# Optimization experiments

Measured on AMD Instinct MI355X. Metric: run time of the kernel, lower is better.

Reference implementation:

```python
import jax, jax.numpy as jnp
import numpy as np

N_NODES = 50000
N_EDGES = 800000
D_IN = 16


def gcn_conv(x, edge_index, W, b, n_nodes):
    """PyG GCNConv: x' = D^{-1/2} (A + I) D^{-1/2} X W + b (add_self_loops=True)."""
    h = x @ W  # [N, d_out] - transform before propagate (small d => cheaper)
    src = jnp.concatenate([edge_index[0], jnp.arange(n_nodes)])  # add self-loops
    dst = jnp.concatenate([edge_index[1], jnp.arange(n_nodes)])
    deg = jax.ops.segment_sum(jnp.ones_like(dst, dtype=h.dtype), dst,
                              num_segments=n_nodes)  # in-degree incl. self-loop
    deg_inv_sqrt = jnp.where(deg > 0, jax.lax.rsqrt(deg), 0.0)
    norm = deg_inv_sqrt[src] * deg_inv_sqrt[dst]  # [E+N]
    msg = h[src] * norm[:, None]                  # gather + scale
    out = jax.ops.segment_sum(msg, dst, num_segments=n_nodes)  # scatter-add
    return out + b


def setup_inputs() -> dict:
    key = jax.random.key(0)
    ks = jax.random.split(key, 16)
    d = D_IN
    x = jax.random.normal(ks[0], (N_NODES, d), dtype=jnp.float32)
    edge_index = jax.random.randint(ks[1], (2, N_EDGES), 0, N_NODES, dtype=jnp.int64)

    def glorot(k, fan_in, fan_out):
        s = (6.0 / (fan_in + fan_out)) ** 0.5
        return jax.random.uniform(k, (fan_in, fan_out), jnp.float32, -s, s)

    return {
        "x": x,
        "edge_index": edge_index,
        "W1": glorot(ks[2], d, 2 * d),      "b1": jnp.zeros((2 * d,), jnp.float32),
        "W2": glorot(ks[3], 2 * d, 4 * d),  "b2": jnp.zeros((4 * d,), jnp.float32),
        "W3": glorot(ks[4], 4 * d, 8 * d),  "b3": jnp.zeros((8 * d,), jnp.float32),
        "Wl1": glorot(ks[5], 8 * d, 4 * d), "bl1": jnp.zeros((4 * d,), jnp.float32),
        "Wl2": glorot(ks[6], 4 * d, 2 * d), "bl2": jnp.zeros((2 * d,), jnp.float32),
        "Wl3": glorot(ks[7], 2 * d, d),     "bl3": jnp.zeros((d,), jnp.float32),
    }


def reference(x, edge_index, W1, b1, W2, b2, W3, b3, Wl1, bl1, Wl2, bl2, Wl3, bl3):
    n = x.shape[0]
    # note: original applies relu twice per conv; relu is idempotent
    out = jax.nn.relu(gcn_conv(x, edge_index, W1, b1, n))
    out = jax.nn.relu(gcn_conv(out, edge_index, W2, b2, n))
    out = jax.nn.relu(gcn_conv(out, edge_index, W3, b3, n))
    out = jax.nn.relu(out @ Wl1 + bl1)
    out = jax.nn.relu(out @ Wl2 + bl2)
    out = jax.nn.relu(out @ Wl3 + bl3)
    return out
```

## Files before the change

kernel.cpp:

```cpp
#include <hip/hip_runtime.h>

#define TPB 256
#define TE  2048
#define MAXB 6144

typedef _Float16 half_t;
typedef _Float16 half4 __attribute__((ext_vector_type(4)));
typedef _Float16 half8 __attribute__((ext_vector_type(8)));
typedef float float8v __attribute__((ext_vector_type(8)));

static inline int cdiv(int a, int b) { return (a + b - 1) / b; }


__global__ void k_zero_int(int* p, int n) {
    int i = blockIdx.x * blockDim.x + threadIdx.x;
    if (i < n) p[i] = 0;
}

__global__ void k_bhist(const int* __restrict__ dst, int* __restrict__ gcnt,
                        int e, int nb) {
    __shared__ int lc[256];
    for (int t = threadIdx.x; t < nb; t += TPB) lc[t] = 0;
    __syncthreads();
    for (int i = blockIdx.x * TPB + threadIdx.x; i < e; i += gridDim.x * TPB)
        atomicAdd(&lc[dst[i] >> 8], 1);
    __syncthreads();
    for (int t = threadIdx.x; t < nb; t += TPB) {
        int v = lc[t];
        if (v) atomicAdd(&gcnt[t], v);
    }
}

__global__ void k_bscan(const int* __restrict__ gcnt, int* __restrict__ bstart,
                        int* __restrict__ bcur, int nb, int e) {
    __shared__ int s[256];
    int t = threadIdx.x;
    int v = (t < nb) ? gcnt[t] : 0;
    s[t] = v;
    __syncthreads();
    for (int d = 1; d < 256; d <<= 1) {
        int x = (t >= d) ? s[t - d] : 0;
        __syncthreads();
        s[t] += x;
        __syncthreads();
    }
    if (t < nb) { int ex = s[t] - v; bstart[t] = ex; bcur[t] = ex; }
    if (t == 0) bstart[nb] = e;
}

__global__ void __launch_bounds__(TPB)
k_binscatter(const int* __restrict__ src, const int* __restrict__ dst,
             int* __restrict__ bcur, unsigned int* __restrict__ gbuf,
             int e, int nb) {
    __shared__ int lcnt[256], loffs[256], lcur[256], gres[256];
    __shared__ int ss[256];
    __shared__ unsigned int ldata[TE];
    const int base = blockIdx.x * TE;
    const int cnt = min(TE, e - base);
    for (int t = threadIdx.x; t < nb; t += TPB) lcnt[t] = 0;
    __syncthreads();

    unsigned int myv[TE / TPB];
    int myb[TE / TPB];
#pragma unroll
    for (int k = 0; k < TE / TPB; ++k) {
        int j = threadIdx.x + k * TPB;
        if (j < cnt) {
            int d = dst[base + j], s = src[base + j];
            int b = d >> 8;
            myv[k] = ((unsigned)b << 24) | ((unsigned)(d & 255) << 16) | (unsigned)s;
            myb[k] = b;
            atomicAdd(&lcnt[b], 1);
        } else myb[k] = -1;
    }
    __syncthreads();
    {
        int t = threadIdx.x;
        int v = (t < nb) ? lcnt[t] : 0;
        ss[t] = v;
        __syncthreads();
        for (int d = 1; d < 256; d <<= 1) {
            int x = (t >= d) ? ss[t - d] : 0;
            __syncthreads();
            ss[t] += x;
            __syncthreads();
        }
        if (t < nb) { loffs[t] = ss[t] - v; lcur[t] = ss[t] - v; }
    }
    __syncthreads();
    for (int t = threadIdx.x; t < nb; t += TPB)
        if (lcnt[t]) gres[t] = atomicAdd(&bcur[t], lcnt[t]);
#pragma unroll
    for (int k = 0; k < TE / TPB; ++k) {
        if (myb[k] >= 0) {
            int p = atomicAdd(&lcur[myb[k]], 1);
            ldata[p] = myv[k];
        }
    }
    __syncthreads();
    for (int j = threadIdx.x; j < cnt; j += TPB) {
        unsigned int v = ldata[j];
        int b = v >> 24;
        gbuf[gres[b] + (j - loffs[b])] = v & 0xFFFFFFu;
    }
}

__global__ void __launch_bounds__(TPB)
k_csr(const unsigned int* __restrict__ gbuf, const int* __restrict__ bstart,
      int* __restrict__ offs, float* __restrict__ dinv, int* __restrict__ ssrc,
      int n, int e) {
    __shared__ int cnt[256], loffs2[256], lcur2[256], ss[256];
    __shared__ int stage[MAXB];
    const int b = blockIdx.x;
    const int s0 = bstart[b], s1 = bstart[b + 1];
    const int m = s1 - s0;
    cnt[threadIdx.x] = 0;
    __syncthreads();
    for (int j = threadIdx.x; j < m; j += TPB)
        atomicAdd(&cnt[(gbuf[s0 + j] >> 16) & 255], 1);
    __syncthreads();
    {
        int t = threadIdx.x;
        int v = cnt[t];
        ss[t] = v;
        __syncthreads();
        for (int d = 1; d < 256; d <<= 1) {
            int x = (t >= d) ? ss[t - d] : 0;
            __syncthreads();
            ss[t] += x;
            __syncthreads();
        }
        loffs2[t] = ss[t] - v;
        lcur2[t] = ss[t] - v;
        int node = b * 256 + t;
        if (node < n) {
            offs[node] = s0 + loffs2[t];
            dinv[node] = rsqrtf((float)v + 1.0f);
        }
    }
    __syncthreads();
    for (int j = threadIdx.x; j < m; j += TPB) {
        unsigned int v = gbuf[s0 + j];
        int p = atomicAdd(&lcur2[(v >> 16) & 255], 1);
        stage[p] = (int)(v & 0xFFFFu);
    }
    __syncthreads();
    for (int j = threadIdx.x; j < m; j += TPB) ssrc[s0 + j] = stage[j];
    if (b == 0 && threadIdx.x == 0) offs[n] = e;
}


__global__ void k_scale(const float* __restrict__ x, const float* __restrict__ dinv,
                        half_t* __restrict__ G, int n) {
    int idx = blockIdx.x * blockDim.x + threadIdx.x;
    if (idx >= n * 2) return;
    float d = dinv[idx >> 1];
    float8v v = ((const float8v*)x)[idx];
    half8 h;
#pragma unroll
    for (int q = 0; q < 8; ++q) h[q] = (half_t)(v[q] * d);
    ((half8*)G)[idx] = h;
}

template<int D>
__global__ void __launch_bounds__(TPB)
k_gather(const int* __restrict__ offs, const int* __restrict__ ssrc,
         const half_t* __restrict__ G, const float* __restrict__ dinv,
         float* __restrict__ A, int n) {
    constexpr int C = D / 8;
    int idx = blockIdx.x * blockDim.x + threadIdx.x;
    if (idx >= n * C) return;
    int i = idx / C;
    int c = idx & (C - 1);
    const half8* Grow = (const half8*)G;
    half8 hs = Grow[(size_t)i * C + c];
    float8v acc;
#pragma unroll
    for (int q = 0; q < 8; ++q) acc[q] = (float)hs[q];
    int s0 = offs[i], s1 = offs[i + 1];
    int j = s0;
    for (; j + 1 < s1; j += 2) {
        int sa = ssrc[j], sb = ssrc[j + 1];
        half8 ga = Grow[(size_t)sa * C + c];
        half8 gb = Grow[(size_t)sb * C + c];
#pragma unroll
        for (int q = 0; q < 8; ++q) acc[q] += (float)ga[q] + (float)gb[q];
    }
    if (j < s1) {
        half8 ga = Grow[(size_t)ssrc[j] * C + c];
#pragma unroll
        for (int q = 0; q < 8; ++q) acc[q] += (float)ga[q];
    }
    float di = dinv[i];
#pragma unroll
    for (int q = 0; q < 8; ++q) acc[q] *= di;
    ((float8v*)A)[(size_t)i * C + c] = acc;
}

template<int DI, int DO, int R, bool SCALE, bool OUT_HALF>
__global__ void __launch_bounds__(TPB, 2)
k_gemm(const float* __restrict__ A, const float* __restrict__ W,
       const float* __restrict__ b, const float* __restrict__ dinv,
       void* __restrict__ outp, int n) {
    constexpr int CT = DO / 4;
    constexpr int RT = TPB / CT;
    constexpr int TM = RT * R;
    constexpr int K4 = DI / 4;
    constexpr int PX = K4 + 1;
    __shared__ float4 sW4[DI * CT];
    __shared__ float4 sX4[TM * PX];
    const int tid = threadIdx.x;

    const float4* Wg = (const float4*)W;
    for (int t = tid; t < DI * CT; t += TPB) sW4[t] = Wg[t];

    const int r0 = blockIdx.x * TM;
    const float4* Ag = (const float4*)A;
    for (int t = tid; t < TM * K4; t += TPB) {
        int r = t / K4, k4 = t - r * K4;
        int row = r0 + r;
        sX4[r * PX + k4] = (row < n) ? Ag[(size_t)row * K4 + k4]
                                     : make_float4(0.f, 0.f, 0.f, 0.f);
    }
    __syncthreads();

    const int c = tid & (CT - 1);
    const int rg = tid / CT;
    const int rbase = rg * R;
    float4 acc[R];
#pragma unroll
    for (int r = 0; r < R; ++r) acc[r] = make_float4(0.f, 0.f, 0.f, 0.f);

#pragma unroll 2
    for (int k4 = 0; k4 < K4; ++k4) {
        float4 xv[R];
#pragma unroll
        for (int r = 0; r < R; ++r) xv[r] = sX4[(rbase + r) * PX + k4];
#pragma unroll
        for (int kk = 0; kk < 4; ++kk) {
            float4 wv = sW4[(k4 * 4 + kk) * CT + c];
#pragma unroll
            for (int r = 0; r < R; ++r) {
                float xs = (kk == 0) ? xv[r].x : (kk == 1) ? xv[r].y
                         : (kk == 2) ? xv[r].z : xv[r].w;
                acc[r].x += xs * wv.x; acc[r].y += xs * wv.y;
                acc[r].z += xs * wv.z; acc[r].w += xs * wv.w;
            }
        }
    }

    float4 bc = ((const float4*)b)[c];
#pragma unroll
    for (int r = 0; r < R; ++r) {
        int row = r0 + rbase + r;
        if (row < n) {
            float4 o;
            o.x = fmaxf(acc[r].x + bc.x, 0.f);
            o.y = fmaxf(acc[r].y + bc.y, 0.f);
            o.z = fmaxf(acc[r].z + bc.z, 0.f);
            o.w = fmaxf(acc[r].w + bc.w, 0.f);
            if (SCALE) {
                float d = dinv[row];
                o.x *= d; o.y *= d; o.z *= d; o.w *= d;
            }
            if (OUT_HALF) {
                half4 h;
                h.x = (half_t)o.x; h.y = (half_t)o.y;
                h.z = (half_t)o.z; h.w = (half_t)o.w;
                ((half4*)outp)[(size_t)row * CT + c] = h;
            } else {
                ((float4*)outp)[(size_t)row * CT + c] = o;
            }
        }
    }
}

extern "C" void kernel_launch(void* const* d_in, const int* in_sizes, int n_in,
                              void* d_out, int out_size, void* d_ws, size_t ws_size,
                              hipStream_t stream) {
    const float* x   = (const float*)d_in[0];
    const int*   ei  = (const int*)d_in[1];
    const float* W1  = (const float*)d_in[2];
    const float* bb1 = (const float*)d_in[3];
    const float* W2  = (const float*)d_in[4];
    const float* bb2 = (const float*)d_in[5];
    const float* W3  = (const float*)d_in[6];
    const float* bb3 = (const float*)d_in[7];
    const float* Wl1 = (const float*)d_in[8];
    const float* bl1 = (const float*)d_in[9];
    const float* Wl2 = (const float*)d_in[10];
    const float* bl2 = (const float*)d_in[11];
    const float* Wl3 = (const float*)d_in[12];
    const float* bl3 = (const float*)d_in[13];
    float* out = (float*)d_out;

    const int n = in_sizes[0] / 16;
    const int e = in_sizes[1] / 2;
    const int* src = ei;
    const int* dst = ei + e;
    const int nb = cdiv(n, 256);

    char* p = (char*)d_ws;
    auto alloc = [&](size_t bytes) {
        char* r = p;
        p += (bytes + 255) & ~(size_t)255;
        return r;
    };
    float*        dinv   = (float*)        alloc((size_t)n * 4);
    int*          offs   = (int*)          alloc((size_t)(n + 1) * 4);
    int*          gcnt   = (int*)          alloc(256 * 4);
    int*          bstart = (int*)          alloc(257 * 4);
    int*          bcur   = (int*)          alloc(256 * 4);
    unsigned int* gbuf   = (unsigned int*) alloc((size_t)e * 4);
    int*          ssrc   = (int*)          alloc((size_t)e * 4);
    half_t*       H1     = (half_t*)       alloc((size_t)n * 64 * 2);
    half_t*       H2     = (half_t*)       alloc((size_t)n * 64 * 2);
    float*        A      = (float*)        alloc((size_t)n * 64 * 4);
    float*        X3     = (float*)        alloc((size_t)n * 128 * 4);
    float*        T1     = A;
    float*        T2     = (float*)H1;

    k_zero_int<<<1, 256, 0, stream>>>(gcnt, nb);
    k_bhist<<<512, TPB, 0, stream>>>(dst, gcnt, e, nb);
    k_bscan<<<1, 256, 0, stream>>>(gcnt, bstart, bcur, nb, e);
    k_binscatter<<<cdiv(e, TE), TPB, 0, stream>>>(src, dst, bcur, gbuf, e, nb);
    k_csr<<<nb, TPB, 0, stream>>>(gbuf, bstart, offs, dinv, ssrc, n, e);

    k_scale<<<cdiv(n * 2, TPB), TPB, 0, stream>>>(x, dinv, H1, n);
    k_gather<16><<<cdiv(n * 2, TPB), TPB, 0, stream>>>(offs, ssrc, H1, dinv, A, n);
    k_gemm<16, 32, 4, true, true><<<cdiv(n, 128), TPB, 0, stream>>>(A, W1, bb1, dinv, H2, n);

    k_gather<32><<<cdiv(n * 4, TPB), TPB, 0, stream>>>(offs, ssrc, H2, dinv, A, n);
    k_gemm<32, 64, 4, true, true><<<cdiv(n, 64), TPB, 0, stream>>>(A, W2, bb2, dinv, H1, n);

    k_gather<64><<<cdiv(n * 8, TPB), TPB, 0, stream>>>(offs, ssrc, H1, dinv, A, n);
    k_gemm<64, 128, 4, false, false><<<cdiv(n, 32), TPB, 0, stream>>>(A, W3, bb3, nullptr, X3, n);

    k_gemm<128, 64, 2, false, false><<<cdiv(n, 32), TPB, 0, stream>>>(X3, Wl1, bl1, nullptr, T1, n);
    k_gemm<64, 32, 2, false, false><<<cdiv(n, 64), TPB, 0, stream>>>(T1, Wl2, bl2, nullptr, T2, n);
    k_gemm<32, 16, 2, false, false><<<cdiv(n, 128), TPB, 0, stream>>>(T2, Wl3, bl3, nullptr, out, n);
}
```

Measured before the change: 231.6 us.

## Fuse neighbor gather into conv GEMM and fuse three MLP head layers

Each GCN layer's gather-aggregate now runs inside the GEMM kernel: every thread aggregates one 8-wide chunk of a row straight into shared memory, so the fp32 intermediate A is never written to or read back from global memory. The third conv now writes fp16 output, and a new fused head kernel runs all three linear+ReLU layers per 64-row tile with fp16 weights in shared memory. This drops several launches and large fp32 round trips. In exchange, the gather now runs with the GEMM tiling and occupancy, and the head layers lose some precision from the fp16 storage.

```diff
diff --git a/kernel.cpp b/kernel.cpp
--- a/kernel.cpp
+++ b/kernel.cpp
@@ -162,65 +162,59 @@
     ((half8*)G)[idx] = h;
 }
 
-template<int D>
-__global__ void __launch_bounds__(TPB)
-k_gather(const int* __restrict__ offs, const int* __restrict__ ssrc,
-         const half_t* __restrict__ G, const float* __restrict__ dinv,
-         float* __restrict__ A, int n) {
-    constexpr int C = D / 8;
-    int idx = blockIdx.x * blockDim.x + threadIdx.x;
-    if (idx >= n * C) return;
-    int i = idx / C;
-    int c = idx & (C - 1);
-    const half8* Grow = (const half8*)G;
-    half8 hs = Grow[(size_t)i * C + c];
-    float8v acc;
-#pragma unroll
-    for (int q = 0; q < 8; ++q) acc[q] = (float)hs[q];
-    int s0 = offs[i], s1 = offs[i + 1];
-    int j = s0;
-    for (; j + 1 < s1; j += 2) {
-        int sa = ssrc[j], sb = ssrc[j + 1];
-        half8 ga = Grow[(size_t)sa * C + c];
-        half8 gb = Grow[(size_t)sb * C + c];
-#pragma unroll
-        for (int q = 0; q < 8; ++q) acc[q] += (float)ga[q] + (float)gb[q];
-    }
-    if (j < s1) {
-        half8 ga = Grow[(size_t)ssrc[j] * C + c];
-#pragma unroll
-        for (int q = 0; q < 8; ++q) acc[q] += (float)ga[q];
-    }
-    float di = dinv[i];
-#pragma unroll
-    for (int q = 0; q < 8; ++q) acc[q] *= di;
-    ((float8v*)A)[(size_t)i * C + c] = acc;
-}
-
 template<int DI, int DO, int R, bool SCALE, bool OUT_HALF>
 __global__ void __launch_bounds__(TPB, 2)
-k_gemm(const float* __restrict__ A, const float* __restrict__ W,
-       const float* __restrict__ b, const float* __restrict__ dinv,
+k_conv(const int* __restrict__ offs, const int* __restrict__ ssrc,
+       const half_t* __restrict__ G, const float* __restrict__ dinv,
+       const float* __restrict__ W, const float* __restrict__ b,
        void* __restrict__ outp, int n) {
     constexpr int CT = DO / 4;
     constexpr int RT = TPB / CT;
     constexpr int TM = RT * R;
     constexpr int K4 = DI / 4;
     constexpr int PX = K4 + 1;
+    constexpr int C  = DI / 8;
+    static_assert(TM * C == TPB, "gather/gemm tile mismatch");
     __shared__ float4 sW4[DI * CT];
     __shared__ float4 sX4[TM * PX];
     const int tid = threadIdx.x;
+    const int r0 = blockIdx.x * TM;
 
     const float4* Wg = (const float4*)W;
     for (int t = tid; t < DI * CT; t += TPB) sW4[t] = Wg[t];
 
-    const int r0 = blockIdx.x * TM;
-    const float4* Ag = (const float4*)A;
-    for (int t = tid; t < TM * K4; t += TPB) {
-        int r = t / K4, k4 = t - r * K4;
-        int row = r0 + r;
-        sX4[r * PX + k4] = (row < n) ? Ag[(size_t)row * K4 + k4]
-                                     : make_float4(0.f, 0.f, 0.f, 0.f);
+    {
+        int gr = tid / C;
+        int gc = tid - gr * C;
+        int row = r0 + gr;
+        float8v acc;
+#pragma unroll
+        for (int q = 0; q < 8; ++q) acc[q] = 0.f;
+        if (row < n) {
+            const half8* Grow = (const half8*)G;
+            half8 hs = Grow[(size_t)row * C + gc];
+#pragma unroll
+            for (int q = 0; q < 8; ++q) acc[q] = (float)hs[q];
+            int s0 = offs[row], s1 = offs[row + 1];
+            int j = s0;
+            for (; j + 1 < s1; j += 2) {
+                int sa = ssrc[j], sb = ssrc[j + 1];
+                half8 ga = Grow[(size_t)sa * C + gc];
+                half8 gb = Grow[(size_t)sb * C + gc];
+#pragma unroll
+                for (int q = 0; q < 8; ++q) acc[q] += (float)ga[q] + (float)gb[q];
+            }
+            if (j < s1) {
+                half8 ga = Grow[(size_t)ssrc[j] * C + gc];
+#pragma unroll
+                for (int q = 0; q < 8; ++q) acc[q] += (float)ga[q];
+            }
+            float di = dinv[row];
+#pragma unroll
+            for (int q = 0; q < 8; ++q) acc[q] *= di;
+        }
+        sX4[gr * PX + 2 * gc]     = make_float4(acc[0], acc[1], acc[2], acc[3]);
+        sX4[gr * PX + 2 * gc + 1] = make_float4(acc[4], acc[5], acc[6], acc[7]);
     }
     __syncthreads();
 
@@ -271,6 +265,122 @@
             } else {
                 ((float4*)outp)[(size_t)row * CT + c] = o;
             }
+        }
+    }
+}
+
+__global__ void __launch_bounds__(256, 2)
+k_head(const half_t* __restrict__ X,
+       const float* __restrict__ W1, const float* __restrict__ b1,
+       const float* __restrict__ W2, const float* __restrict__ b2,
+       const float* __restrict__ W3, const float* __restrict__ b3,
+       float* __restrict__ out, int n) {
+    __shared__ half_t hW1[128 * 64];
+    __shared__ half_t hW2[64 * 32];
+    __shared__ half_t hW3[32 * 16];
+    __shared__ float h1[64 * 65];
+    __shared__ float h2[64 * 33];
+    const int tid = threadIdx.x;
+    const int r0 = blockIdx.x * 64;
+
+    for (int t = tid; t < 128 * 64; t += 256) hW1[t] = (half_t)W1[t];
+    for (int t = tid; t < 64 * 32; t += 256) hW2[t] = (half_t)W2[t];
+    for (int t = tid; t < 32 * 16; t += 256) hW3[t] = (half_t)W3[t];
+    __syncthreads();
+
+    {
+        const int c4 = tid & 15;
+        const int rowg = tid >> 4;
+        const half8* Xr = (const half8*)X;
+        float acc[4][4];
+#pragma unroll
+        for (int r = 0; r < 4; ++r)
+#pragma unroll
+            for (int j = 0; j < 4; ++j) acc[r][j] = 0.f;
+        for (int k8 = 0; k8 < 16; ++k8) {
+            half8 xh[4];
+#pragma unroll
+            for (int r = 0; r < 4; ++r) {
+                int row = r0 + rowg * 4 + r;
+                if (row < n) xh[r] = Xr[(size_t)row * 16 + k8];
+                else { half8 z; for (int q = 0; q < 8; ++q) z[q] = (half_t)0.f; xh[r] = z; }
+            }
+#pragma unroll
+            for (int q = 0; q < 8; ++q) {
+                int k = k8 * 8 + q;
+                half4 w = *(const half4*)&hW1[k * 64 + c4 * 4];
+                float w0 = (float)w.x, w1 = (float)w.y, w2 = (float)w.z, w3 = (float)w.w;
+#pragma unroll
+                for (int r = 0; r < 4; ++r) {
+                    float xs = (float)xh[r][q];
+                    acc[r][0] += xs * w0; acc[r][1] += xs * w1;
+                    acc[r][2] += xs * w2; acc[r][3] += xs * w3;
+                }
+            }
+        }
+        float4 bc = ((const float4*)b1)[c4];
+#pragma unroll
+        for (int r = 0; r < 4; ++r) {
+            int rl = rowg * 4 + r;
+            h1[rl * 65 + c4 * 4 + 0] = fmaxf(acc[r][0] + bc.x, 0.f);
+            h1[rl * 65 + c4 * 4 + 1] = fmaxf(acc[r][1] + bc.y, 0.f);
+            h1[rl * 65 + c4 * 4 + 2] = fmaxf(acc[r][2] + bc.z, 0.f);
+            h1[rl * 65 + c4 * 4 + 3] = fmaxf(acc[r][3] + bc.w, 0.f);
+        }
+    }
+    __syncthreads();
+
+    {
+        const int c4 = tid & 7;
+        const int rowg = tid >> 3;
+        float acc[2][4];
+#pragma unroll
+        for (int r = 0; r < 2; ++r)
+#pragma unroll
+            for (int j = 0; j < 4; ++j) acc[r][j] = 0.f;
+#pragma unroll 4
+        for (int k = 0; k < 64; ++k) {
+            half4 w = *(const half4*)&hW2[k * 32 + c4 * 4];
+            float w0 = (float)w.x, w1 = (float)w.y, w2 = (float)w.z, w3 = (float)w.w;
+#pragma unroll
+            for (int r = 0; r < 2; ++r) {
+                float xs = h1[(rowg * 2 + r) * 65 + k];
+                acc[r][0] += xs * w0; acc[r][1] += xs * w1;
+                acc[r][2] += xs * w2; acc[r][3] += xs * w3;
+            }
+        }
+        float4 bc = ((const float4*)b2)[c4];
+#pragma unroll
+        for (int r = 0; r < 2; ++r) {
+            int rl = rowg * 2 + r;
+            h2[rl * 33 + c4 * 4 + 0] = fmaxf(acc[r][0] + bc.x, 0.f);
+            h2[rl * 33 + c4 * 4 + 1] = fmaxf(acc[r][1] + bc.y, 0.f);
+            h2[rl * 33 + c4 * 4 + 2] = fmaxf(acc[r][2] + bc.z, 0.f);
+            h2[rl * 33 + c4 * 4 + 3] = fmaxf(acc[r][3] + bc.w, 0.f);
+        }
+    }
+    __syncthreads();
+
+    {
+        const int c4 = tid & 3;
+        const int rl = tid >> 2;
+        float a0 = 0.f, a1 = 0.f, a2 = 0.f, a3 = 0.f;
+#pragma unroll 4
+        for (int k = 0; k < 32; ++k) {
+            half4 w = *(const half4*)&hW3[k * 16 + c4 * 4];
+            float xs = h2[rl * 33 + k];
+            a0 += xs * (float)w.x; a1 += xs * (float)w.y;
+            a2 += xs * (float)w.z; a3 += xs * (float)w.w;
+        }
+        int row = r0 + rl;
+        if (row < n) {
+            float4 bc = ((const float4*)b3)[c4];
+            float4 o;
+            o.x = fmaxf(a0 + bc.x, 0.f);
+            o.y = fmaxf(a1 + bc.y, 0.f);
+            o.z = fmaxf(a2 + bc.z, 0.f);
+            o.w = fmaxf(a3 + bc.w, 0.f);
+            ((float4*)out)[(size_t)row * 4 + c4] = o;
         }
     }
 }
@@ -314,11 +424,8 @@
     unsigned int* gbuf   = (unsigned int*) alloc((size_t)e * 4);
     int*          ssrc   = (int*)          alloc((size_t)e * 4);
     half_t*       H1     = (half_t*)       alloc((size_t)n * 64 * 2);
-    half_t*       H2     = (half_t*)       alloc((size_t)n * 64 * 2);
-    float*        A      = (float*)        alloc((size_t)n * 64 * 4);
-    float*        X3     = (float*)        alloc((size_t)n * 128 * 4);
-    float*        T1     = A;
-    float*        T2     = (float*)H1;
+    half_t*       H2     = (half_t*)       alloc((size_t)n * 32 * 2);
+    half_t*       X3h    = (half_t*)       alloc((size_t)n * 128 * 2);
 
     k_zero_int<<<1, 256, 0, stream>>>(gcnt, nb);
     k_bhist<<<512, TPB, 0, stream>>>(dst, gcnt, e, nb);
@@ -327,16 +434,12 @@
     k_csr<<<nb, TPB, 0, stream>>>(gbuf, bstart, offs, dinv, ssrc, n, e);
 
     k_scale<<<cdiv(n * 2, TPB), TPB, 0, stream>>>(x, dinv, H1, n);
-    k_gather<16><<<cdiv(n * 2, TPB), TPB, 0, stream>>>(offs, ssrc, H1, dinv, A, n);
-    k_gemm<16, 32, 4, true, true><<<cdiv(n, 128), TPB, 0, stream>>>(A, W1, bb1, dinv, H2, n);
-
-    k_gather<32><<<cdiv(n * 4, TPB), TPB, 0, stream>>>(offs, ssrc, H2, dinv, A, n);
-    k_gemm<32, 64, 4, true, true><<<cdiv(n, 64), TPB, 0, stream>>>(A, W2, bb2, dinv, H1, n);
-
-    k_gather<64><<<cdiv(n * 8, TPB), TPB, 0, stream>>>(offs, ssrc, H1, dinv, A, n);
-    k_gemm<64, 128, 4, false, false><<<cdiv(n, 32), TPB, 0, stream>>>(A, W3, bb3, nullptr, X3, n);
-
-    k_gemm<128, 64, 2, false, false><<<cdiv(n, 32), TPB, 0, stream>>>(X3, Wl1, bl1, nullptr, T1, n);
-    k_gemm<64, 32, 2, false, false><<<cdiv(n, 64), TPB, 0, stream>>>(T1, Wl2, bl2, nullptr, T2, n);
-    k_gemm<32, 16, 2, false, false><<<cdiv(n, 128), TPB, 0, stream>>>(T2, Wl3, bl3, nullptr, out, n);
-}
+    k_conv<16, 32, 4, true, true><<<cdiv(n, 128), TPB, 0, stream>>>(
+        offs, ssrc, H1, dinv, W1, bb1, H2, n);
+    k_conv<32, 64, 4, true, true><<<cdiv(n, 64), TPB, 0, stream>>>(
+        offs, ssrc, H2, dinv, W2, bb2, H1, n);
+    k_conv<64, 128, 4, false, true><<<cdiv(n, 32), TPB, 0, stream>>>(
+        offs, ssrc, H1, dinv, W3, bb3, X3h, n);
+
+    k_head<<<cdiv(n, 64), 256, 0, stream>>>(X3h, Wl1, bl1, Wl2, bl2, Wl3, bl3, out, n);
+}
```

Measured after the change: 230.8 us. No clear change (-0.3%).
